# Kernel optimization log

Measured on AMD Instinct MI355X. Metric: run time of the kernel, lower is better.

## Reference

```python
import jax, jax.numpy as jnp
import numpy as np

B, S, H = 8, 1024, 16
DV = 1024      # video_input_dim
LAT = 1024     # latent_dim
DQ = LAT // H  # query_dim = 64
DH = 64        # head_dim


def setup_inputs() -> dict:
    key = jax.random.key(0)
    ks = jax.random.split(key, 12)
    sc = lambda fan_in: 1.0 / np.sqrt(fan_in)
    return {
        "input": jax.random.normal(ks[0], (B, S, DV), jnp.float32),
        "latent": jax.random.normal(ks[1], (B, S, LAT), jnp.float32),
        "attention_mask": jax.random.randint(ks[2], (B * H, S, S), 0, 2, jnp.int32),
        "Wq": jax.random.normal(ks[3], (LAT, H * DQ), jnp.float32) * sc(LAT),
        "bq": jnp.zeros((H * DQ,), jnp.float32),
        "Wk": jax.random.normal(ks[4], (DV, H * DQ), jnp.float32) * sc(DV),
        "bk": jnp.zeros((H * DQ,), jnp.float32),
        "Wv": jax.random.normal(ks[5], (DV, H * DH), jnp.float32) * sc(DV),
        "bv": jnp.zeros((H * DH,), jnp.float32),
        "Wo": jax.random.normal(ks[6], (H * DH, LAT), jnp.float32) * sc(H * DH),
        "bo": jnp.zeros((LAT,), jnp.float32),
    }


def reference(input, latent, attention_mask, Wq, bq, Wk, bk, Wv, bv, Wo, bo):
    b, s, _ = input.shape
    # projections -> [b, h, s, d]
    q = (latent @ Wq + bq).reshape(b, s, H, DQ).transpose(0, 2, 1, 3)
    k = (input @ Wk + bk).reshape(b, s, H, DQ).transpose(0, 2, 1, 3)
    v = (input @ Wv + bv).reshape(b, s, H, DH).transpose(0, 2, 1, 3)
    # [b, h, s, s] score matrix (materialized, as in the original bmm)
    scores = jnp.einsum("bhqd,bhkd->bhqk", q, k) / jnp.sqrt(jnp.float32(DQ))
    mask = attention_mask.reshape(b, H, s, s)
    scores = jnp.where(mask == 0, -jnp.inf, scores)
    weights = jax.nn.softmax(scores, axis=-1)
    out = jnp.einsum("bhqk,bhkd->bhqd", weights, v)  # [b, h, s, dh]
    out = out.transpose(0, 2, 1, 3).reshape(b, s, H * DH)
    return out @ Wo + bo
```

## Files before the change

### kernel.cpp

```cpp
#include <hip/hip_runtime.h>
#include <hip/hip_bf16.h>
#include <stdint.h>

typedef __bf16 bf16;
typedef __bf16 bf16x8 __attribute__((ext_vector_type(8)));
typedef float f32x4 __attribute__((ext_vector_type(4)));
typedef unsigned short u16;
typedef unsigned short u16x4 __attribute__((ext_vector_type(4)));


__device__ __forceinline__ void gld16(const bf16* g, bf16* l) {
    __builtin_amdgcn_global_load_lds(
        (const __attribute__((address_space(1))) void*)g,
        (__attribute__((address_space(3))) void*)l, 16, 0, 0);
}

__global__ void convert_f32_bf16(const float* __restrict__ s0, bf16* __restrict__ d0,
                                 const float* __restrict__ s1, bf16* __restrict__ d1) {
    const float* src = blockIdx.y ? s1 : s0;
    bf16* dst = blockIdx.y ? d1 : d0;
    const int nchunk = (8 * 1024 * 1024) / 4;
    for (int c = blockIdx.x * blockDim.x + threadIdx.x; c < nchunk;
         c += gridDim.x * blockDim.x) {
        float4 v = *(const float4*)&src[(size_t)c * 4];
        u16x4 o;
        o[0] = __builtin_bit_cast(u16, (bf16)v.x);
        o[1] = __builtin_bit_cast(u16, (bf16)v.y);
        o[2] = __builtin_bit_cast(u16, (bf16)v.z);
        o[3] = __builtin_bit_cast(u16, (bf16)v.w);
        *(u16x4*)&dst[(size_t)c * 4] = o;
    }
}

__global__ void transpose4(const float* __restrict__ w0, const float* __restrict__ w1,
                           const float* __restrict__ w2, const float* __restrict__ w3,
                           bf16* __restrict__ t0, bf16* __restrict__ t1,
                           bf16* __restrict__ t2, bf16* __restrict__ t3) {
    __shared__ float tile[32][33];
    const float* src; bf16* dst;
    switch (blockIdx.z) {
        case 0:  src = w0; dst = t0; break;
        case 1:  src = w1; dst = t1; break;
        case 2:  src = w2; dst = t2; break;
        default: src = w3; dst = t3; break;
    }
    int tx = threadIdx.x, ty = threadIdx.y;
    int x = blockIdx.x * 32 + tx;
    int y = blockIdx.y * 32 + ty;
    #pragma unroll
    for (int j = 0; j < 32; j += 8)
        tile[ty + j][tx] = src[(size_t)(y + j) * 1024 + x];
    __syncthreads();
    int x2 = blockIdx.y * 32 + tx;
    int y2 = blockIdx.x * 32 + ty;
    #pragma unroll
    for (int j = 0; j < 32; j += 8)
        dst[(size_t)(y2 + j) * 1024 + x2] = (bf16)tile[tx][ty + j];
}

template<int MODE>
__global__ __launch_bounds__(256) void gemm_bt(const bf16* __restrict__ X,
                                               const bf16* __restrict__ Wt,
                                               const float* __restrict__ bias,
                                               void* __restrict__ outv) {
    __shared__ bf16 Al[128 * 32];
    __shared__ bf16 Bl[128 * 32];
    const int tid  = threadIdx.x;
    const int m0   = blockIdx.x * 128;
    const int n0   = blockIdx.y * 128;
    const int lane = tid & 63;
    const int w    = tid >> 6;
    const int wm   = (w & 1) * 64;
    const int wn   = (w >> 1) * 64;
    const int l15  = lane & 15;
    const int quad = lane >> 4;
    const int sw   = (l15 >> 1) & 3;

    f32x4 acc[4][4] = {};

    for (int kt = 0; kt < 1024; kt += 32) {
        __syncthreads();
        #pragma unroll
        for (int t = 0; t < 2; t++) {
            int c = (w * 2 + t) * 64 + lane;
            int row = c >> 2;
            int e   = (c & 3) ^ ((c >> 3) & 3);
            gld16(&X [(size_t)(m0 + row) * 1024 + kt + e * 8], &Al[(w * 2 + t) * 512]);
            gld16(&Wt[(size_t)(n0 + row) * 1024 + kt + e * 8], &Bl[(w * 2 + t) * 512]);
        }
        __syncthreads();
        bf16x8 a[4], b[4];
        #pragma unroll
        for (int i = 0; i < 4; i++)
            a[i] = *(const bf16x8*)&Al[(wm + i * 16 + l15) * 32 + (quad ^ sw) * 8];
        #pragma unroll
        for (int j = 0; j < 4; j++)
            b[j] = *(const bf16x8*)&Bl[(wn + j * 16 + l15) * 32 + (quad ^ sw) * 8];
        #pragma unroll
        for (int i = 0; i < 4; i++)
            #pragma unroll
            for (int j = 0; j < 4; j++)
                acc[i][j] = __builtin_amdgcn_mfma_f32_16x16x32_bf16(a[i], b[j], acc[i][j], 0, 0, 0);
    }

    float bv[4];
    #pragma unroll
    for (int j = 0; j < 4; j++) bv[j] = bias[n0 + wn + j * 16 + l15];

    #pragma unroll
    for (int i = 0; i < 4; i++) {
        int mbase = m0 + wm + i * 16 + quad * 4;
        #pragma unroll
        for (int j = 0; j < 4; j++) {
            int n = n0 + wn + j * 16 + l15;
            if (MODE == 2) {
                bf16* out = (bf16*)outv;
                int b = mbase >> 10, s = mbase & 1023;
                int h = n >> 6, d = n & 63;
                u16x4 pack;
                #pragma unroll
                for (int r = 0; r < 4; r++) {
                    bf16 v = (bf16)(acc[i][j][r] + bv[j]);
                    pack[r] = __builtin_bit_cast(u16, v);
                }
                *(u16x4*)&out[(((size_t)(b * 16 + h)) * 64 + d) * 1024 + s] = pack;
            } else if (MODE == 1) {
                bf16* out = (bf16*)outv;
                #pragma unroll
                for (int r = 0; r < 4; r++) {
                    int m = mbase + r;
                    int b = m >> 10, s = m & 1023;
                    int h = n >> 6, d = n & 63;
                    out[(((size_t)(b * 16 + h)) * 1024 + s) * 64 + d] =
                        (bf16)(acc[i][j][r] + bv[j]);
                }
            } else {
                float* out = (float*)outv;
                #pragma unroll
                for (int r = 0; r < 4; r++)
                    out[(size_t)(mbase + r) * 1024 + n] = acc[i][j][r] + bv[j];
            }
        }
    }
}

__global__ __launch_bounds__(256, 2) void attn(const bf16* __restrict__ Q,
                                               const bf16* __restrict__ K,
                                               const bf16* __restrict__ Vt,
                                               const int*  __restrict__ mask,
                                               bf16* __restrict__ O) {
    __shared__ bf16 Kl[2][4096];
    __shared__ bf16 Vl[2][4096];
    __shared__ bf16 Pl[4][32 * 68];

    const int tid  = threadIdx.x;
    const int lane = tid & 63;
    const int w    = tid >> 6;
    const int l15  = lane & 15;
    const int quad = lane >> 4;

    const int blk = blockIdx.x;
    const int bh  = (blk & 7) * 16 + (blk >> 6);
    const int q0  = ((blk >> 3) & 7) * 128;
    const int qrow0 = q0 + w * 32;

    const bf16* Kbh = K  + (size_t)bh * 65536;
    const bf16* Vbh = Vt + (size_t)bh * 65536;
    const int* mbase = mask + ((size_t)bh * 1024 + qrow0 + quad * 4) * 1024;

    bf16x8 qa[2][2];
    #pragma unroll
    for (int rb = 0; rb < 2; rb++) {
        const bf16* Qb = Q + ((size_t)bh * 1024 + qrow0 + rb * 16 + l15) * 64;
        qa[rb][0] = *(const bf16x8*)&Qb[quad * 8];
        qa[rb][1] = *(const bf16x8*)&Qb[32 + quad * 8];
    }

    const int c0 = (w * 2 + 0) * 64 + lane;
    const int c1 = (w * 2 + 1) * 64 + lane;
    const int swz = l15 & 7;

    #define STAGE_KV(kk, buf)                                                          \
        {                                                                              \
            int r0 = c0 >> 3, e0 = (c0 & 7) ^ (r0 & 7);                                \
            int r1 = c1 >> 3, e1 = (c1 & 7) ^ (r1 & 7);                                \
            gld16(&Kbh[(size_t)((kk) + r0) * 64 + e0 * 8], &Kl[buf][(w * 2 + 0) * 512]); \
            gld16(&Kbh[(size_t)((kk) + r1) * 64 + e1 * 8], &Kl[buf][(w * 2 + 1) * 512]); \
            gld16(&Vbh[(size_t)r0 * 1024 + (kk) + e0 * 8], &Vl[buf][(w * 2 + 0) * 512]); \
            gld16(&Vbh[(size_t)r1 * 1024 + (kk) + e1 * 8], &Vl[buf][(w * 2 + 1) * 512]); \
        }

    STAGE_KV(0, 0);
    int mn[2][4][4];
    #pragma unroll
    for (int rb = 0; rb < 2; rb++)
        #pragma unroll
        for (int r = 0; r < 4; r++)
            #pragma unroll
            for (int t = 0; t < 4; t++)
                mn[rb][r][t] = mbase[(size_t)(rb * 16 + r) * 1024 + t * 16 + l15];

    f32x4 o[2][4] = {};
    float lsum[2][4] = {};
    bf16* Pw = Pl[w];

    for (int it = 0; it < 16; it++) {
        __syncthreads();
        const int cur = it & 1, nxt = cur ^ 1;
        const int kn = ((it + 1) & 15) * 64;

        int nib[2][4];
        #pragma unroll
        for (int rb = 0; rb < 2; rb++)
            #pragma unroll
            for (int r = 0; r < 4; r++)
                nib[rb][r] = (mn[rb][r][0] != 0) | ((mn[rb][r][1] != 0) << 1) |
                             ((mn[rb][r][2] != 0) << 2) | ((mn[rb][r][3] != 0) << 3);

        STAGE_KV(kn, nxt);
        #pragma unroll
        for (int rb = 0; rb < 2; rb++)
            #pragma unroll
            for (int r = 0; r < 4; r++)
                #pragma unroll
                for (int t = 0; t < 4; t++)
                    mn[rb][r][t] = mbase[(size_t)(rb * 16 + r) * 1024 + kn + t * 16 + l15];

        f32x4 s[2][4];
        #pragma unroll
        for (int t = 0; t < 4; t++) {
            bf16x8 kb0 = *(const bf16x8*)&Kl[cur][(t * 16 + l15) * 64 + ((0 + quad) ^ swz) * 8];
            bf16x8 kb1 = *(const bf16x8*)&Kl[cur][(t * 16 + l15) * 64 + ((4 + quad) ^ swz) * 8];
            #pragma unroll
            for (int rb = 0; rb < 2; rb++) {
                f32x4 z = {};
                z = __builtin_amdgcn_mfma_f32_16x16x32_bf16(qa[rb][0], kb0, z, 0, 0, 0);
                z = __builtin_amdgcn_mfma_f32_16x16x32_bf16(qa[rb][1], kb1, z, 0, 0, 0);
                s[rb][t] = z;
            }
        }

        #pragma unroll
        for (int rb = 0; rb < 2; rb++)
            #pragma unroll
            for (int t = 0; t < 4; t++)
                #pragma unroll
                for (int r = 0; r < 4; r++) {
                    float p = __expf(fmaf(s[rb][t][r], 0.125f, -12.0f));
                    p = ((nib[rb][r] >> t) & 1) ? p : 0.0f;
                    lsum[rb][r] += p;
                    Pw[(rb * 16 + quad * 4 + r) * 68 + t * 16 + l15] = (bf16)p;
                }

        bf16x8 pa[2][2];
        #pragma unroll
        for (int rb = 0; rb < 2; rb++) {
            pa[rb][0] = *(const bf16x8*)&Pw[(rb * 16 + l15) * 68 + quad * 8];
            pa[rb][1] = *(const bf16x8*)&Pw[(rb * 16 + l15) * 68 + 32 + quad * 8];
        }
        #pragma unroll
        for (int nt = 0; nt < 4; nt++) {
            bf16x8 vb0 = *(const bf16x8*)&Vl[cur][(nt * 16 + l15) * 64 + ((0 + quad) ^ swz) * 8];
            bf16x8 vb1 = *(const bf16x8*)&Vl[cur][(nt * 16 + l15) * 64 + ((4 + quad) ^ swz) * 8];
            #pragma unroll
            for (int rb = 0; rb < 2; rb++) {
                o[rb][nt] = __builtin_amdgcn_mfma_f32_16x16x32_bf16(pa[rb][0], vb0, o[rb][nt], 0, 0, 0);
                o[rb][nt] = __builtin_amdgcn_mfma_f32_16x16x32_bf16(pa[rb][1], vb1, o[rb][nt], 0, 0, 0);
            }
        }
    }
    #undef STAGE_KV

    const int b = bh >> 4, h = bh & 15;
    #pragma unroll
    for (int rb = 0; rb < 2; rb++)
        #pragma unroll
        for (int r = 0; r < 4; r++) {
            float l = lsum[rb][r];
            #pragma unroll
            for (int off = 1; off < 16; off <<= 1)
                l += __shfl_xor(l, off, 64);
            float inv = 1.0f / l;
            int srow = qrow0 + rb * 16 + quad * 4 + r;
            bf16* orow = O + ((size_t)(b * 1024 + srow)) * 1024 + h * 64;
            #pragma unroll
            for (int nt = 0; nt < 4; nt++)
                orow[nt * 16 + l15] = (bf16)(o[rb][nt][r] * inv);
        }
}

extern "C" void kernel_launch(void* const* d_in, const int* in_sizes, int n_in,
                              void* d_out, int out_size, void* d_ws, size_t ws_size,
                              hipStream_t stream) {
    const float* input  = (const float*)d_in[0];
    const float* latent = (const float*)d_in[1];
    const int*   mask   = (const int*)d_in[2];
    const float* Wq = (const float*)d_in[3];
    const float* bq = (const float*)d_in[4];
    const float* Wk = (const float*)d_in[5];
    const float* bk = (const float*)d_in[6];
    const float* Wv = (const float*)d_in[7];
    const float* bv = (const float*)d_in[8];
    const float* Wo = (const float*)d_in[9];
    const float* bo = (const float*)d_in[10];
    float* out = (float*)d_out;

    char* ws = (char*)d_ws;
    bf16* Xb  = (bf16*)(ws);
    bf16* Lb  = (bf16*)(ws + (16u << 20));
    bf16* Qh  = (bf16*)(ws + (32u << 20));
    bf16* Kh  = (bf16*)(ws + (48u << 20));
    bf16* Vt  = (bf16*)(ws + (64u << 20));
    bf16* Ob  = (bf16*)(ws + (80u << 20));
    bf16* Wqt = (bf16*)(ws + (96u << 20));
    bf16* Wkt = (bf16*)(ws + (98u << 20));
    bf16* Wvt = (bf16*)(ws + (100u << 20));
    bf16* Wot = (bf16*)(ws + (102u << 20));

    convert_f32_bf16<<<dim3(2048, 2, 1), 256, 0, stream>>>(input, Xb, latent, Lb);

    transpose4<<<dim3(32, 32, 4), dim3(32, 8, 1), 0, stream>>>(
        Wq, Wk, Wv, Wo, Wqt, Wkt, Wvt, Wot);

    dim3 g(64, 8, 1);
    gemm_bt<1><<<g, 256, 0, stream>>>(Lb, Wqt, bq, Qh);
    gemm_bt<1><<<g, 256, 0, stream>>>(Xb, Wkt, bk, Kh);
    gemm_bt<2><<<g, 256, 0, stream>>>(Xb, Wvt, bv, Vt);

    attn<<<dim3(1024, 1, 1), 256, 0, stream>>>(Qh, Kh, Vt, mask, Ob);

    gemm_bt<0><<<g, 256, 0, stream>>>(Ob, Wot, bo, out);
}
```

Baseline: 917.0 us.

## Pre-pack attention mask into bitmasks and stage them into LDS

Adds a separate kernel that reads the int32 mask once, coalesced, and packs each 32-column chunk into a uint32 bitword. The attention kernel then loads these packed bits asynchronously into LDS alongside K/V, instead of issuing many scattered 4-byte global loads of int32 mask values into registers. This removes mask registers and uncoalesced loads and raises the occupancy target to 3 blocks. The full 512MB mask is still read, now by an extra pass plus a small packed-buffer write and reread.

Result: slower. 988.6 us (+7.8%).

```diff
diff --git a/kernel.cpp b/kernel.cpp
--- a/kernel.cpp
+++ b/kernel.cpp
@@ -9,7 +9,7 @@
 typedef unsigned short u16x4 __attribute__((ext_vector_type(4)));
 
 
-__device__ __forceinline__ void gld16(const bf16* g, bf16* l) {
+__device__ __forceinline__ void gld16(const void* g, void* l) {
     __builtin_amdgcn_global_load_lds(
         (const __attribute__((address_space(1))) void*)g,
         (__attribute__((address_space(3))) void*)l, 16, 0, 0);
@@ -30,6 +30,26 @@
         o[3] = __builtin_bit_cast(u16, (bf16)v.w);
         *(u16x4*)&dst[(size_t)c * 4] = o;
     }
+}
+
+__global__ __launch_bounds__(256) void pack_mask(const int* __restrict__ mask,
+                                                 uint32_t* __restrict__ pk) {
+    int gid = blockIdx.x * 256 + threadIdx.x;
+    int w  = gid & 1;
+    int s  = (gid >> 1) & 1023;
+    int it = (gid >> 11) & 15;
+    int bh = gid >> 15;
+    const int* src = mask + ((size_t)bh * 1024 + s) * 1024 + it * 64 + w * 32;
+    uint32_t bits = 0;
+    #pragma unroll
+    for (int c = 0; c < 8; c++) {
+        int4 v = *(const int4*)&src[c * 4];
+        bits |= (v.x != 0 ? 1u : 0u) << (c * 4 + 0);
+        bits |= (v.y != 0 ? 1u : 0u) << (c * 4 + 1);
+        bits |= (v.z != 0 ? 1u : 0u) << (c * 4 + 2);
+        bits |= (v.w != 0 ? 1u : 0u) << (c * 4 + 3);
+    }
+    pk[gid] = bits;
 }
 
 __global__ void transpose4(const float* __restrict__ w0, const float* __restrict__ w1,
@@ -144,14 +164,15 @@
     }
 }
 
-__global__ __launch_bounds__(256, 2) void attn(const bf16* __restrict__ Q,
+__global__ __launch_bounds__(256, 3) void attn(const bf16* __restrict__ Q,
                                                const bf16* __restrict__ K,
                                                const bf16* __restrict__ Vt,
-                                               const int*  __restrict__ mask,
+                                               const uint32_t* __restrict__ pk,
                                                bf16* __restrict__ O) {
     __shared__ bf16 Kl[2][4096];
     __shared__ bf16 Vl[2][4096];
     __shared__ bf16 Pl[4][32 * 68];
+    __shared__ uint32_t Ml[2][256];
 
     const int tid  = threadIdx.x;
     const int lane = tid & 63;
@@ -166,7 +187,7 @@
 
     const bf16* Kbh = K  + (size_t)bh * 65536;
     const bf16* Vbh = Vt + (size_t)bh * 65536;
-    const int* mbase = mask + ((size_t)bh * 1024 + qrow0 + quad * 4) * 1024;
+    const uint32_t* pkb = pk + ((size_t)bh * 16 * 1024 + q0) * 2;
 
     bf16x8 qa[2][2];
     #pragma unroll
@@ -180,25 +201,19 @@
     const int c1 = (w * 2 + 1) * 64 + lane;
     const int swz = l15 & 7;
 
-    #define STAGE_KV(kk, buf)                                                          \
+    #define STAGE_KV(itx, buf)                                                         \
         {                                                                              \
+            int kk = (itx) * 64;                                                       \
             int r0 = c0 >> 3, e0 = (c0 & 7) ^ (r0 & 7);                                \
             int r1 = c1 >> 3, e1 = (c1 & 7) ^ (r1 & 7);                                \
-            gld16(&Kbh[(size_t)((kk) + r0) * 64 + e0 * 8], &Kl[buf][(w * 2 + 0) * 512]); \
-            gld16(&Kbh[(size_t)((kk) + r1) * 64 + e1 * 8], &Kl[buf][(w * 2 + 1) * 512]); \
-            gld16(&Vbh[(size_t)r0 * 1024 + (kk) + e0 * 8], &Vl[buf][(w * 2 + 0) * 512]); \
-            gld16(&Vbh[(size_t)r1 * 1024 + (kk) + e1 * 8], &Vl[buf][(w * 2 + 1) * 512]); \
+            gld16(&Kbh[(size_t)(kk + r0) * 64 + e0 * 8], &Kl[buf][(w * 2 + 0) * 512]); \
+            gld16(&Kbh[(size_t)(kk + r1) * 64 + e1 * 8], &Kl[buf][(w * 2 + 1) * 512]); \
+            gld16(&Vbh[(size_t)r0 * 1024 + kk + e0 * 8], &Vl[buf][(w * 2 + 0) * 512]); \
+            gld16(&Vbh[(size_t)r1 * 1024 + kk + e1 * 8], &Vl[buf][(w * 2 + 1) * 512]); \
+            if (w == 0) gld16(&pkb[(itx) * 2048 + lane * 4], &Ml[buf][0]);             \
         }
 
     STAGE_KV(0, 0);
-    int mn[2][4][4];
-    #pragma unroll
-    for (int rb = 0; rb < 2; rb++)
-        #pragma unroll
-        for (int r = 0; r < 4; r++)
-            #pragma unroll
-            for (int t = 0; t < 4; t++)
-                mn[rb][r][t] = mbase[(size_t)(rb * 16 + r) * 1024 + t * 16 + l15];
 
     f32x4 o[2][4] = {};
     float lsum[2][4] = {};
@@ -207,24 +222,8 @@
     for (int it = 0; it < 16; it++) {
         __syncthreads();
         const int cur = it & 1, nxt = cur ^ 1;
-        const int kn = ((it + 1) & 15) * 64;
-
-        int nib[2][4];
-        #pragma unroll
-        for (int rb = 0; rb < 2; rb++)
-            #pragma unroll
-            for (int r = 0; r < 4; r++)
-                nib[rb][r] = (mn[rb][r][0] != 0) | ((mn[rb][r][1] != 0) << 1) |
-                             ((mn[rb][r][2] != 0) << 2) | ((mn[rb][r][3] != 0) << 3);
-
-        STAGE_KV(kn, nxt);
-        #pragma unroll
-        for (int rb = 0; rb < 2; rb++)
-            #pragma unroll
-            for (int r = 0; r < 4; r++)
-                #pragma unroll
-                for (int t = 0; t < 4; t++)
-                    mn[rb][r][t] = mbase[(size_t)(rb * 16 + r) * 1024 + kn + t * 16 + l15];
+
+        STAGE_KV((it + 1) & 15, nxt);
 
         f32x4 s[2][4];
         #pragma unroll
@@ -243,14 +242,17 @@
         #pragma unroll
         for (int rb = 0; rb < 2; rb++)
             #pragma unroll
-            for (int t = 0; t < 4; t++)
+            for (int r = 0; r < 4; r++) {
+                uint2 mwv = *(const uint2*)&Ml[cur][(w * 32 + rb * 16 + quad * 4 + r) * 2];
                 #pragma unroll
-                for (int r = 0; r < 4; r++) {
+                for (int t = 0; t < 4; t++) {
+                    uint32_t wd = (t & 2) ? mwv.y : mwv.x;
                     float p = __expf(fmaf(s[rb][t][r], 0.125f, -12.0f));
-                    p = ((nib[rb][r] >> t) & 1) ? p : 0.0f;
+                    p = ((wd >> ((t & 1) * 16 + l15)) & 1) ? p : 0.0f;
                     lsum[rb][r] += p;
                     Pw[(rb * 16 + quad * 4 + r) * 68 + t * 16 + l15] = (bf16)p;
                 }
+            }
 
         bf16x8 pa[2][2];
         #pragma unroll
@@ -316,18 +318,21 @@
     bf16* Wkt = (bf16*)(ws + (98u << 20));
     bf16* Wvt = (bf16*)(ws + (100u << 20));
     bf16* Wot = (bf16*)(ws + (102u << 20));
+    uint32_t* pk = (uint32_t*)(ws + (104u << 20));
 
     convert_f32_bf16<<<dim3(2048, 2, 1), 256, 0, stream>>>(input, Xb, latent, Lb);
 
     transpose4<<<dim3(32, 32, 4), dim3(32, 8, 1), 0, stream>>>(
         Wq, Wk, Wv, Wo, Wqt, Wkt, Wvt, Wot);
+
+    pack_mask<<<dim3(16384, 1, 1), 256, 0, stream>>>(mask, pk);
 
     dim3 g(64, 8, 1);
     gemm_bt<1><<<g, 256, 0, stream>>>(Lb, Wqt, bq, Qh);
     gemm_bt<1><<<g, 256, 0, stream>>>(Xb, Wkt, bk, Kh);
     gemm_bt<2><<<g, 256, 0, stream>>>(Xb, Wvt, bv, Vt);
 
-    attn<<<dim3(1024, 1, 1), 256, 0, stream>>>(Qh, Kh, Vt, mask, Ob);
+    attn<<<dim3(1024, 1, 1), 256, 0, stream>>>(Qh, Kh, Vt, pk, Ob);
 
     gemm_bt<0><<<g, 256, 0, stream>>>(Ob, Wot, bo, out);
 }
```
